# Kernel optimization log

Measured on AMD Instinct MI355X. Metric: run time of the kernel, lower is better.

## Reference

```python
import jax, jax.numpy as jnp
import numpy as np

H, D = 4, 32
DIM = H * D      # hidden_dim * heads = 128
L = 2            # num_layers
F = 1000         # functions per graph
BINS = 16
T = 16           # tensor_neurons
BOTT = 16        # bottle_neck_neurons


def _hgt(xd, xi, especs, Wk, bk, Wq, bq, Wv, bv, Wa, ba, sk, ar, mr, pr):
    # One HGTConv: per-type K/Q/V linears, per-relation head matrices a_rel/m_rel,
    # joint segment-softmax over all incoming edges per dst node, sum-aggregate,
    # gelu -> per-type out linear -> sigmoid-skip residual.
    xt = {"data": xd, "inst": xi}
    Ns = {"data": xd.shape[0], "inst": xi.shape[0]}
    ti = {"data": 0, "inst": 1}

    def proj(W, b):
        return {t: (xt[t] @ W[ti[t]] + b[ti[t]]).reshape(Ns[t], H, D) for t in xt}

    k, q, v = proj(Wk, bk), proj(Wq, bq), proj(Wv, bv)
    buckets = {"data": [], "inst": []}
    for st, dt, ei, r in especs:
        src, dst = ei[0], ei[1]
        krel = jnp.einsum("ehd,hdf->ehf", k[st][src], ar[r])        # [E,H,D]
        logit = (q[dt][dst] * krel).sum(-1) * (pr[r] / (D ** 0.5))   # [E,H]
        vrel = jnp.einsum("ehd,hdf->ehf", v[st][src], mr[r])        # [E,H,D]
        buckets[dt].append((logit, dst, vrel))
    out = {}
    for t in ("data", "inst"):
        logits = jnp.concatenate([b[0] for b in buckets[t]], 0)
        dst = jnp.concatenate([b[1] for b in buckets[t]], 0)
        msgs = jnp.concatenate([b[2] for b in buckets[t]], 0)
        mx = jax.lax.stop_gradient(jax.ops.segment_max(logits, dst, num_segments=Ns[t]))
        e = jnp.exp(logits - mx[dst])
        den = jax.ops.segment_sum(e, dst, num_segments=Ns[t])
        w = e / jnp.maximum(den[dst], 1e-16)
        agg = jax.ops.segment_sum(msgs * w[..., None], dst, num_segments=Ns[t]).reshape(Ns[t], DIM)
        o = jax.nn.gelu(agg) @ Wa[ti[t]] + ba[ti[t]]
        s = jax.nn.sigmoid(sk[ti[t]])
        out[t] = s * o + (1.0 - s) * xt[t]
    return out["data"], out["inst"]


def _conv_pass(xd, xi, edges, P):
    Wk, bk, Wq, bq, Wv, bv, Wa, ba, sk, ar, mr, pr = P
    ec, ein, eou, eca = edges
    for l in range(L):
        fe = [("inst", "inst", ec, 0), ("data", "inst", ein, 1),
              ("inst", "data", eou, 2), ("inst", "inst", eca, 3)]
        re = [("inst", "inst", ec[::-1], 0), ("inst", "data", ein[::-1], 1),
              ("data", "inst", eou[::-1], 2), ("inst", "inst", eca[::-1], 3)]
        p0 = [A[l, 0] for A in (Wk, bk, Wq, bq, Wv, bv, Wa, ba, sk, ar, mr, pr)]
        p1 = [A[l, 1] for A in (Wk, bk, Wq, bq, Wv, bv, Wa, ba, sk, ar, mr, pr)]
        d1, i1 = _hgt(xd, xi, fe, *p0)
        d2, i2 = _hgt(xd, xi, re, *p1)
        xd = jax.nn.relu(0.5 * d1 + 0.5 * d2)   # alpha = 0.5
        xi = jax.nn.relu(0.5 * i1 + 0.5 * i2)
    return xd, xi


def _att_pool(x, W_att):
    # SimGNN AttentionModule
    c = jnp.tanh(jnp.mean(x @ W_att, axis=0))
    s = jax.nn.sigmoid(x @ c)
    return x.T @ s  # [DIM]


def _func_pool(xd, xi, fd, fi, W_att):
    # per-function attention pooling via segment ops (cat(data,inst) per function)
    x = jnp.concatenate([xd, xi], 0)
    f = jnp.concatenate([fd, fi], 0)
    sums = jax.ops.segment_sum(x @ W_att, f, num_segments=F)
    cnt = jax.ops.segment_sum(jnp.ones((x.shape[0],), jnp.float32), f, num_segments=F)
    c = jnp.tanh(sums / jnp.maximum(cnt, 1.0)[:, None])
    s = jax.nn.sigmoid((x * c[f]).sum(-1))
    return jax.ops.segment_sum(x * s[:, None], f, num_segments=F)  # [F,DIM]


def _forward(g1_x_data, g1_x_inst, g2_x_data, g2_x_inst, W_k, b_k, W_q, b_q, W_v, b_v,
             W_a, b_a, skip, a_rel, m_rel, p_rel, W_att, W_tn, V_tn, b_tn, W_fc1, b_fc1,
             W_sc, b_sc, g1_ei_control, g1_ei_input, g1_ei_output, g1_ei_call,
             g1_func_data, g1_func_inst, g2_ei_control, g2_ei_input, g2_ei_output,
             g2_ei_call, g2_func_data, g2_func_inst):
    P = (W_k, b_k, W_q, b_q, W_v, b_v, W_a, b_a, skip, a_rel, m_rel, p_rel)
    d1, i1 = _conv_pass(g1_x_data, g1_x_inst, (g1_ei_control, g1_ei_input, g1_ei_output, g1_ei_call), P)
    d2, i2 = _conv_pass(g2_x_data, g2_x_inst, (g2_ei_control, g2_ei_input, g2_ei_output, g2_ei_call), P)
    f1 = _func_pool(d1, i1, g1_func_data, g1_func_inst, W_att)
    f2 = _func_pool(d2, i2, g2_func_data, g2_func_inst, W_att)
    # histogram of detached similarity scores (torch.histc over [min,max])
    sc = jax.lax.stop_gradient(f1 @ f2.T).reshape(-1)
    mn, mx = sc.min(), sc.max()
    idx = jnp.clip(jnp.floor((sc - mn) / jnp.maximum(mx - mn, 1e-12) * BINS).astype(jnp.int32), 0, BINS - 1)
    hist = jax.ops.segment_sum(jnp.ones_like(sc), idx, num_segments=BINS)
    hist = hist / hist.sum()
    p1 = _att_pool(jnp.concatenate([d1, i1], 0), W_att)
    p2 = _att_pool(jnp.concatenate([d2, i2], 0), W_att)
    scoring = jnp.einsum("i,ijk,j->k", p1, W_tn, p2)          # NTN bilinear [T]
    block = V_tn @ jnp.concatenate([p1, p2]) + b_tn
    tnet = jax.nn.relu(scoring + block)
    feats = jnp.concatenate([tnet, hist])[None, :]             # [1, T+BINS]
    h = jax.nn.relu(feats @ W_fc1 + b_fc1)
    return jax.nn.sigmoid(h @ W_sc + b_sc)                     # [1,1]


def setup_inputs():
    key = jax.random.key(0)
    ks = iter(jax.random.split(key, 80))
    Nd, Ni = 30000, 60000
    Ec, Ein, Eou, Eca = 120000, 90000, 90000, 30000

    def nrm(shape, s):
        return jax.random.normal(next(ks), shape, jnp.float32) * s

    def ri(n, hi):
        return jax.random.randint(next(ks), (n,), 0, hi, jnp.int32)

    inp = {}
    for g in ("g1", "g2"):
        inp[g + "_x_data"] = nrm((Nd, DIM), 1.0)
        inp[g + "_x_inst"] = nrm((Ni, DIM), 1.0)
        inp[g + "_ei_control"] = jnp.stack([ri(Ec, Ni), ri(Ec, Ni)])
        inp[g + "_ei_input"] = jnp.stack([ri(Ein, Nd), ri(Ein, Ni)])
        inp[g + "_ei_output"] = jnp.stack([ri(Eou, Ni), ri(Eou, Nd)])
        inp[g + "_ei_call"] = jnp.stack([ri(Eca, Ni), ri(Eca, Ni)])
        inp[g + "_func_data"] = (jnp.arange(Nd) % F).astype(jnp.int32)
        inp[g + "_func_inst"] = (jnp.arange(Ni) % F).astype(jnp.int32)
    w = 1.0 / (DIM ** 0.5)
    for nm in ("k", "q", "v", "a"):
        inp["W_" + nm] = nrm((L, 2, 2, DIM, DIM), w)
        inp["b_" + nm] = jnp.zeros((L, 2, 2, DIM), jnp.float32)
    inp["skip"] = jnp.ones((L, 2, 2), jnp.float32)
    inp["a_rel"] = nrm((L, 2, 4, H, D, D), 1.0 / (D ** 0.5))
    inp["m_rel"] = nrm((L, 2, 4, H, D, D), 1.0 / (D ** 0.5))
    inp["p_rel"] = jnp.ones((L, 2, 4, H), jnp.float32)
    inp["W_att"] = nrm((DIM, DIM), w)
    inp["W_tn"] = nrm((DIM, DIM, T), w)
    inp["V_tn"] = nrm((T, 2 * DIM), w)
    inp["b_tn"] = jnp.zeros((T,), jnp.float32)
    inp["W_fc1"] = nrm((T + BINS, BOTT), 0.1)
    inp["b_fc1"] = jnp.zeros((BOTT,), jnp.float32)
    inp["W_sc"] = nrm((BOTT, 1), 0.1)
    inp["b_sc"] = jnp.zeros((1,), jnp.float32)
    return inp


def reference(g1_x_data, g1_x_inst, g2_x_data, g2_x_inst, W_k, b_k, W_q, b_q, W_v, b_v,
              W_a, b_a, skip, a_rel, m_rel, p_rel, W_att, W_tn, V_tn, b_tn, W_fc1, b_fc1,
              W_sc, b_sc, g1_ei_control, g1_ei_input, g1_ei_output, g1_ei_call,
              g1_func_data, g1_func_inst, g2_ei_control, g2_ei_input, g2_ei_output,
              g2_ei_call, g2_func_data, g2_func_inst):
    return _forward(g1_x_data, g1_x_inst, g2_x_data, g2_x_inst, W_k, b_k, W_q, b_q, W_v, b_v,
                    W_a, b_a, skip, a_rel, m_rel, p_rel, W_att, W_tn, V_tn, b_tn, W_fc1, b_fc1,
                    W_sc, b_sc, g1_ei_control, g1_ei_input, g1_ei_output, g1_ei_call,
                    g1_func_data, g1_func_inst, g2_ei_control, g2_ei_input, g2_ei_output,
                    g2_ei_call, g2_func_data, g2_func_inst)
```

## Files before the change

### kernel.cpp

```cpp
#include <hip/hip_runtime.h>
#include <math.h>

#define FFUNC 1000

typedef __attribute__((ext_vector_type(8))) short s8v;
typedef __attribute__((ext_vector_type(4))) float f4v;

__device__ __forceinline__ float sigf(float x){ return 1.0f/(1.0f+__expf(-x)); }
__device__ __forceinline__ float geluf(float x){
  float u = 1.5957691216057308f * (x + 0.044715f*x*x*x);
  return x / (1.0f + __expf(-u));
}
__device__ __forceinline__ unsigned fkey(float f){
  unsigned u = __float_as_uint(f);
  return (u & 0x80000000u) ? ~u : (u | 0x80000000u);
}
__device__ __forceinline__ float funkey(unsigned k){
  unsigned u = (k & 0x80000000u) ? (k ^ 0x80000000u) : ~k;
  return __uint_as_float(u);
}
__device__ __forceinline__ void atomAddF(float* p, float v){ unsafeAtomicAdd(p, v); }
__device__ __forceinline__ unsigned short bfr(float x){
  unsigned u = __float_as_uint(x);
  unsigned r = (u + 0x7FFFu + ((u >> 16) & 1u)) >> 16;
  return (unsigned short)r;
}
__device__ __forceinline__ float b2f(unsigned short v){
  return __uint_as_float((unsigned)v << 16);
}

__global__ void packw_k(const float* __restrict__ W, unsigned short* __restrict__ out){
  int mat = blockIdx.x;
  const float* w = W + (size_t)mat*16384;
  unsigned short* o = out + (size_t)mat*16384;
  for (int u=0; u<64; u++){
    int oi = u*256 + threadIdx.x;
    int j = oi & 7, l = (oi>>3) & 63, nt = (oi>>9) & 7, kt = oi >> 12;
    float v = w[(size_t)(kt*32 + 8*(l>>4) + j)*128 + nt*16 + (l&15)];
    o[oi] = bfr(v);
  }
}

__global__ void packa_k(const float* __restrict__ A, unsigned short* __restrict__ out){
  int ent = blockIdx.x;
  const float* a = A + (size_t)ent*4096;
  unsigned short* o = out + (size_t)ent*4096;
  for (int u=0; u<16; u++){
    int oi = u*256 + threadIdx.x;
    int j = oi & 7, l = (oi>>3) & 63, nt = (oi>>9) & 1, h = oi >> 10;
    float v = a[(size_t)h*1024 + (size_t)(8*(l>>4)+j)*32 + nt*16 + (l&15)];
    o[oi] = bfr(v);
  }
}

struct KX { int styp[4]; int koff[4]; };
__global__ __launch_bounds__(256) void gemm_kqvx_k(
    const void* __restrict__ xdv, const void* __restrict__ xiv, int af32,
    int nd, int ni, int gbd,
    const unsigned short* __restrict__ WK, const unsigned short* __restrict__ WQ,
    const unsigned short* __restrict__ WV,
    const float* __restrict__ bK, const float* __restrict__ bQ, const float* __restrict__ bV,
    const unsigned short* __restrict__ ARpc, const unsigned short* __restrict__ MRpc,
    unsigned short* __restrict__ Qb,
    unsigned short* __restrict__ KRK, unsigned short* __restrict__ KRV, KX kx)
{
  __shared__ __align__(16) unsigned short tile[64*128];
  int blk = blockIdx.x;
  int ty = (blk >= gbd);
  int N = ty ? ni : nd;
  int rbase = (ty ? (blk - gbd) : blk) * 64;
  size_t obase = ty ? (size_t)nd*128 : 0;
  const unsigned short* wk = WK + (ty ? 16384 : 0);
  const unsigned short* wq = WQ + (ty ? 16384 : 0);
  const unsigned short* wv = WV + (ty ? 16384 : 0);
  const float* bk2 = bK + (ty ? 128 : 0);
  const float* bq2 = bQ + (ty ? 128 : 0);
  const float* bv2 = bV + (ty ? 128 : 0);
  const float* Af = (const float*)(ty ? xiv : xdv);
  const unsigned short* Ab = (const unsigned short*)(ty ? xiv : xdv);

  int t = threadIdx.x;
  int l = t & 63, w = t >> 6, b = l >> 4, m = l & 15;
  int arow = rbase + w*16 + m;
  bool rv = arow < N;
  int lrow = w*16 + m;

  s8v axf[4];
  #pragma unroll
  for (int kt=0; kt<4; kt++){
    s8v af = (s8v){0,0,0,0,0,0,0,0};
    if (rv){
      if (af32){
        const float* ap = Af + (size_t)arow*128 + kt*32 + b*8;
        float4 x0 = *(const float4*)ap;
        float4 x1 = *(const float4*)(ap + 4);
        af[0]=(short)bfr(x0.x); af[1]=(short)bfr(x0.y); af[2]=(short)bfr(x0.z); af[3]=(short)bfr(x0.w);
        af[4]=(short)bfr(x1.x); af[5]=(short)bfr(x1.y); af[6]=(short)bfr(x1.z); af[7]=(short)bfr(x1.w);
      } else {
        af = *(const s8v*)(Ab + (size_t)arow*128 + kt*32 + b*8);
      }
    }
    axf[kt] = af;
  }

  f4v acc[8];
  #pragma unroll
  for (int nt=0; nt<8; nt++) acc[nt] = (f4v){0,0,0,0};
  #pragma unroll
  for (int kt=0; kt<4; kt++)
    #pragma unroll
    for (int nt=0; nt<8; nt++){
      s8v bf = *(const s8v*)(wq + ((kt*8 + nt)*64 + l)*8);
      acc[nt] = __builtin_amdgcn_mfma_f32_16x16x32_bf16(axf[kt], bf, acc[nt], 0, 0, 0);
    }
  #pragma unroll
  for (int r2=0; r2<4; r2++){
    int trow = w*16 + 4*b + r2;
    #pragma unroll
    for (int nt=0; nt<8; nt++){
      int col = nt*16 + m;
      int ch = (col>>3) ^ (trow&15);
      tile[trow*128 + ch*8 + (col&7)] = bfr(acc[nt][r2] + bq2[col]);
    }
  }
  __syncthreads();
  #pragma unroll
  for (int it=0; it<4; it++){
    int idx = it*256 + t;
    int rr = idx >> 4, cc = idx & 15;
    int orow = rbase + rr;
    if (orow < N)
      *(uint4*)(Qb + obase + (size_t)orow*128 + cc*8) =
          *(const uint4*)(&tile[rr*128 + ((cc ^ (rr&15))*8)]);
  }
  __syncthreads();

  #pragma unroll
  for (int nt=0; nt<8; nt++) acc[nt] = (f4v){0,0,0,0};
  #pragma unroll
  for (int kt=0; kt<4; kt++)
    #pragma unroll
    for (int nt=0; nt<8; nt++){
      s8v bf = *(const s8v*)(wk + ((kt*8 + nt)*64 + l)*8);
      acc[nt] = __builtin_amdgcn_mfma_f32_16x16x32_bf16(axf[kt], bf, acc[nt], 0, 0, 0);
    }
  #pragma unroll
  for (int r2=0; r2<4; r2++){
    int trow = w*16 + 4*b + r2;
    #pragma unroll
    for (int nt=0; nt<8; nt++){
      int col = nt*16 + m;
      int ch = (col>>3) ^ (trow&15);
      tile[trow*128 + ch*8 + (col&7)] = bfr(acc[nt][r2] + bk2[col]);
    }
  }
  __syncthreads();
  {
    s8v kf[4];
    #pragma unroll
    for (int h=0; h<4; h++){
      int ch = (h*4 + b) ^ (lrow&15);
      kf[h] = *(const s8v*)(&tile[lrow*128 + ch*8]);
    }
    __syncthreads();
    #pragma unroll
    for (int r=0; r<4; r++){
      if (kx.styp[r] != ty) continue;
      const unsigned short* Ap = ARpc + r*4096;
      f4v xa[8];
      #pragma unroll
      for (int i=0;i<8;i++) xa[i] = (f4v){0,0,0,0};
      #pragma unroll
      for (int h=0; h<4; h++)
        #pragma unroll
        for (int n2=0; n2<2; n2++){
          s8v bf = *(const s8v*)(Ap + ((h*2 + n2)*64 + l)*8);
          xa[h*2+n2] = __builtin_amdgcn_mfma_f32_16x16x32_bf16(kf[h], bf, xa[h*2+n2], 0, 0, 0);
        }
      #pragma unroll
      for (int r2=0; r2<4; r2++){
        int trow = w*16 + 4*b + r2;
        #pragma unroll
        for (int h=0; h<4; h++)
          #pragma unroll
          for (int n2=0; n2<2; n2++){
            int col = h*32 + n2*16 + m;
            int ch = (col>>3) ^ (trow&15);
            tile[trow*128 + ch*8 + (col&7)] = bfr(xa[h*2+n2][r2]);
          }
      }
      __syncthreads();
      int ko = kx.koff[r];
      #pragma unroll
      for (int it=0; it<4; it++){
        int idx = it*256 + t;
        int rr = idx >> 4, cc = idx & 15;
        int orow = rbase + rr;
        if (orow < N)
          *(uint4*)(KRK + (size_t)(ko + orow)*128 + cc*8) =
              *(const uint4*)(&tile[rr*128 + ((cc ^ (rr&15))*8)]);
      }
      __syncthreads();
    }
  }

  #pragma unroll
  for (int nt=0; nt<8; nt++) acc[nt] = (f4v){0,0,0,0};
  #pragma unroll
  for (int kt=0; kt<4; kt++)
    #pragma unroll
    for (int nt=0; nt<8; nt++){
      s8v bf = *(const s8v*)(wv + ((kt*8 + nt)*64 + l)*8);
      acc[nt] = __builtin_amdgcn_mfma_f32_16x16x32_bf16(axf[kt], bf, acc[nt], 0, 0, 0);
    }
  #pragma unroll
  for (int r2=0; r2<4; r2++){
    int trow = w*16 + 4*b + r2;
    #pragma unroll
    for (int nt=0; nt<8; nt++){
      int col = nt*16 + m;
      int ch = (col>>3) ^ (trow&15);
      tile[trow*128 + ch*8 + (col&7)] = bfr(acc[nt][r2] + bv2[col]);
    }
  }
  __syncthreads();
  {
    s8v vf[4];
    #pragma unroll
    for (int h=0; h<4; h++){
      int ch = (h*4 + b) ^ (lrow&15);
      vf[h] = *(const s8v*)(&tile[lrow*128 + ch*8]);
    }
    __syncthreads();
    #pragma unroll
    for (int r=0; r<4; r++){
      if (kx.styp[r] != ty) continue;
      const unsigned short* Ap = MRpc + r*4096;
      f4v xa[8];
      #pragma unroll
      for (int i=0;i<8;i++) xa[i] = (f4v){0,0,0,0};
      #pragma unroll
      for (int h=0; h<4; h++)
        #pragma unroll
        for (int n2=0; n2<2; n2++){
          s8v bf = *(const s8v*)(Ap + ((h*2 + n2)*64 + l)*8);
          xa[h*2+n2] = __builtin_amdgcn_mfma_f32_16x16x32_bf16(vf[h], bf, xa[h*2+n2], 0, 0, 0);
        }
      #pragma unroll
      for (int r2=0; r2<4; r2++){
        int trow = w*16 + 4*b + r2;
        #pragma unroll
        for (int h=0; h<4; h++)
          #pragma unroll
          for (int n2=0; n2<2; n2++){
            int col = h*32 + n2*16 + m;
            int ch = (col>>3) ^ (trow&15);
            tile[trow*128 + ch*8 + (col&7)] = bfr(xa[h*2+n2][r2]);
          }
      }
      __syncthreads();
      int ko = kx.koff[r];
      #pragma unroll
      for (int it=0; it<4; it++){
        int idx = it*256 + t;
        int rr = idx >> 4, cc = idx & 15;
        int orow = rbase + rr;
        if (orow < N)
          *(uint4*)(KRV + (size_t)(ko + orow)*128 + cc*8) =
              *(const uint4*)(&tile[rr*128 + ((cc ^ (rr&15))*8)]);
      }
      __syncthreads();
    }
  }
}

__global__ __launch_bounds__(256) void gemm_epi_k(
    const unsigned short* __restrict__ AGGb, const float* __restrict__ DENb,
    int nd, int ni, int gbd,
    const unsigned short* __restrict__ WA, const float* __restrict__ bA,
    const void* __restrict__ xin_dv, const void* __restrict__ xin_iv, int xf32,
    const unsigned short* __restrict__ o1p, unsigned short* __restrict__ out,
    const float* __restrict__ skp, int mode)
{
  __shared__ __align__(16) float ftile[64*128];
  int blk = blockIdx.x;
  int ty = (blk >= gbd);
  int N = ty ? ni : nd;
  int rbase = (ty ? (blk - gbd) : blk) * 64;
  int goff = ty ? nd : 0;
  const unsigned short* wa = WA + (ty ? 16384 : 0);
  const float* ba2 = bA + (ty ? 128 : 0);
  const float* xinF = (const float*)(ty ? xin_iv : xin_dv);
  const unsigned short* xinB = (const unsigned short*)(ty ? xin_iv : xin_dv);
  float s = sigf(skp[ty]), s1 = 1.0f - s;

  int t = threadIdx.x;
  int l = t & 63, w = t >> 6, b = l >> 4, m = l & 15;
  int arow = rbase + w*16 + m;
  bool rv = arow < N;
  f4v acc[8];
  #pragma unroll
  for (int nt=0; nt<8; nt++) acc[nt] = (f4v){0,0,0,0};

  float4 dv4 = make_float4(1.f,1.f,1.f,1.f);
  if (rv){
    size_t grow = (size_t)(goff + arow);
    float4 dr = *(const float4*)(DENb + grow*4);
    dv4.x = 1.0f / fmaxf(dr.x, 1e-16f);
    dv4.y = 1.0f / fmaxf(dr.y, 1e-16f);
    dv4.z = 1.0f / fmaxf(dr.z, 1e-16f);
    dv4.w = 1.0f / fmaxf(dr.w, 1e-16f);
  }
  #pragma unroll
  for (int kt=0; kt<4; kt++){
    s8v af = (s8v){0,0,0,0,0,0,0,0};
    if (rv){
      size_t grow = (size_t)(goff + arow);
      float dv = (kt==0)?dv4.x:(kt==1)?dv4.y:(kt==2)?dv4.z:dv4.w;
      s8v ag = *(const s8v*)(AGGb + grow*128 + kt*32 + b*8);
      #pragma unroll
      for (int jj=0; jj<8; jj++)
        af[jj] = (short)bfr(geluf(b2f((unsigned short)ag[jj]) * dv));
    }
    #pragma unroll
    for (int nt=0; nt<8; nt++){
      s8v bf = *(const s8v*)(wa + ((kt*8 + nt)*64 + l)*8);
      acc[nt] = __builtin_amdgcn_mfma_f32_16x16x32_bf16(af, bf, acc[nt], 0, 0, 0);
    }
  }
  #pragma unroll
  for (int r2=0; r2<4; r2++){
    int trow = w*16 + 4*b + r2;
    #pragma unroll
    for (int nt=0; nt<8; nt++){
      int col = nt*16 + m;
      int ch = (col>>2) ^ (trow&31);
      ftile[trow*128 + ch*4 + (col&3)] = acc[nt][r2];
    }
  }
  __syncthreads();
  #pragma unroll
  for (int it=0; it<8; it++){
    int idx = it*256 + t;
    int rr = idx >> 5, cc = idx & 31;
    int orow = rbase + rr;
    if (orow >= N) continue;
    size_t grow = (size_t)(goff + orow);
    float4 a4 = *(const float4*)(&ftile[rr*128 + ((cc ^ (rr&31))*4)]);
    float4 b4 = *(const float4*)(ba2 + cc*4);
    float xv0, xv1, xv2, xv3;
    if (xf32){
      float4 x4 = *(const float4*)(xinF + (size_t)orow*128 + cc*4);
      xv0=x4.x; xv1=x4.y; xv2=x4.z; xv3=x4.w;
    } else {
      ushort4 x4 = *(const ushort4*)(xinB + (size_t)orow*128 + cc*4);
      xv0=b2f(x4.x); xv1=b2f(x4.y); xv2=b2f(x4.z); xv3=b2f(x4.w);
    }
    float v0 = s*(a4.x + b4.x) + s1*xv0;
    float v1 = s*(a4.y + b4.y) + s1*xv1;
    float v2 = s*(a4.z + b4.z) + s1*xv2;
    float v3 = s*(a4.w + b4.w) + s1*xv3;
    if (mode == 3){
      ushort4 o4 = *(const ushort4*)(o1p + grow*128 + cc*4);
      v0 = fmaxf(0.5f*b2f(o4.x) + 0.5f*v0, 0.f);
      v1 = fmaxf(0.5f*b2f(o4.y) + 0.5f*v1, 0.f);
      v2 = fmaxf(0.5f*b2f(o4.z) + 0.5f*v2, 0.f);
      v3 = fmaxf(0.5f*b2f(o4.w) + 0.5f*v3, 0.f);
    }
    *(ushort4*)(out + grow*128 + cc*4) =
        make_ushort4(bfr(v0), bfr(v1), bfr(v2), bfr(v3));
  }
}

struct ScanDesc { int n[8]; };

struct HD {
  int blk0[9];
  const int* dst[8];
  const int* src[8];
  int E[8];
  int cnto[8];
  int permo[8];
};
__global__ void csr_hist_all_k(HD d, int* __restrict__ cnt){
  int b = blockIdx.x;
  int r = 0;
  while (r < 7 && b >= d.blk0[r+1]) r++;
  int e = (b - d.blk0[r])*256 + threadIdx.x;
  if (e < d.E[r]) atomicAdd(&cnt[d.cnto[r] + d.dst[r][e]], 1);
}
__global__ void csr_fill_all_k(HD d, int* __restrict__ curs, int* __restrict__ perm){
  int b = blockIdx.x;
  int r = 0;
  while (r < 7 && b >= d.blk0[r+1]) r++;
  int e = (b - d.blk0[r])*256 + threadIdx.x;
  if (e < d.E[r]){
    int pos = atomicAdd(&curs[d.cnto[r] + d.dst[r][e]], 1);
    perm[d.permo[r] + pos] = d.src[r][e] | ((r & 3) << 24);
  }
}

__global__ __launch_bounds__(1024) void scan_p1(ScanDesc sd, const int* __restrict__ offs,
                                                int* __restrict__ part, int NO, int MAXT){
  int ent = blockIdx.y, tile = blockIdx.x;
  int n = sd.n[ent];
  int i = tile*1024 + threadIdx.x;
  int v = (i < n) ? offs[(size_t)ent*NO + i] : 0;
  #pragma unroll
  for (int d2=1; d2<64; d2<<=1) v += __shfl_xor(v, d2, 64);
  __shared__ int ws_[16];
  int lane = threadIdx.x & 63, wv = threadIdx.x >> 6;
  if (lane == 0) ws_[wv] = v;
  __syncthreads();
  if (threadIdx.x == 0){
    int s = 0;
    #pragma unroll
    for (int k=0;k<16;k++) s += ws_[k];
    part[ent*MAXT + tile] = s;
  }
}

__global__ __launch_bounds__(1024) void scan_p2(int* __restrict__ part, int MAXT, int nent){
  int tid = threadIdx.x, lane = tid & 63, wv = tid >> 6;
  __shared__ int wsum[16];
  __shared__ int woff[17];
  for (int ent=0; ent<nent; ent++){
    int v = (tid < MAXT) ? part[ent*MAXT + tid] : 0;
    int s = v;
    #pragma unroll
    for (int d2=1; d2<64; d2<<=1){
      int t2 = __shfl_up(s, d2, 64);
      if (lane >= d2) s += t2;
    }
    if (lane == 63) wsum[wv] = s;
    __syncthreads();
    if (wv == 0 && lane < 16){
      int x = wsum[lane];
      #pragma unroll
      for (int d2=1; d2<16; d2<<=1){
        int t2 = __shfl_up(x, d2, 64);
        if (lane >= d2) x += t2;
      }
      woff[lane+1] = x;
      if (lane == 0) woff[0] = 0;
    }
    __syncthreads();
    if (tid < MAXT) part[ent*MAXT + tid] = woff[wv] + s - v;
    __syncthreads();
  }
}

__global__ __launch_bounds__(1024) void scan_p3(ScanDesc sd, int* __restrict__ offs,
                                                int* __restrict__ curs,
                                                const int* __restrict__ part, int NO, int MAXT){
  int ent = blockIdx.y, tile = blockIdx.x;
  int n = sd.n[ent];
  int i = tile*1024 + threadIdx.x;
  int v = (i < n) ? offs[(size_t)ent*NO + i] : 0;
  int lane = threadIdx.x & 63, wv = threadIdx.x >> 6;
  int s = v;
  #pragma unroll
  for (int d2=1; d2<64; d2<<=1){
    int t2 = __shfl_up(s, d2, 64);
    if (lane >= d2) s += t2;
  }
  __shared__ int wsum[16];
  __shared__ int woff[17];
  if (lane == 63) wsum[wv] = s;
  __syncthreads();
  if (wv == 0 && lane < 16){
    int x = wsum[lane];
    #pragma unroll
    for (int d2=1; d2<16; d2<<=1){
      int t2 = __shfl_up(x, d2, 64);
      if (lane >= d2) x += t2;
    }
    woff[lane+1] = x;
    if (lane == 0) woff[0] = 0;
  }
  __syncthreads();
  int excl = part[ent*MAXT + tile] + woff[wv] + s - v;
  if (i < n){
    offs[(size_t)ent*NO + i] = excl;
    curs[(size_t)ent*NO + i] = excl;
  }
  if (i == n-1) offs[(size_t)ent*NO + n] = excl + v;
}

__global__ void fhist_k(const int* __restrict__ fd, const int* __restrict__ fi,
                        int Nd, int Ni, int* __restrict__ cnt){
  int nt = Nd + Ni;
  for (int n = blockIdx.x*256 + threadIdx.x; n < nt; n += gridDim.x*256){
    int f = (n < Nd) ? fd[n] : fi[n-Nd];
    atomicAdd(&cnt[f], 1);
  }
}
__global__ void ffill_k(const int* __restrict__ fd, const int* __restrict__ fi,
                        int Nd, int Ni, int* __restrict__ curs, int* __restrict__ perm){
  int nt = Nd + Ni;
  for (int n = blockIdx.x*256 + threadIdx.x; n < nt; n += gridDim.x*256){
    int f = (n < Nd) ? fd[n] : fi[n-Nd];
    int pos = atomicAdd(&curs[f], 1);
    perm[pos] = n;
  }
}

struct MD { int koff[4]; };
__global__ __launch_bounds__(256) void e12m_k(
    const unsigned short* __restrict__ KRK, const unsigned short* __restrict__ KRV,
    const unsigned short* __restrict__ Qb,
    const int* __restrict__ offs, const int* __restrict__ perm, int nrows,
    const float* __restrict__ pr,
    unsigned short* __restrict__ aggb, float* __restrict__ den, MD md)
{
  int gidx = blockIdx.x*256 + threadIdx.x;
  int node = gidx >> 5; if (node >= nrows) return;
  int sub = gidx & 31, h = sub >> 3, j = sub & 7;
  int o0 = offs[node], o1 = offs[node+1];
  unsigned short* ap = aggb + (size_t)node*128 + h*32 + j*4;
  if (o0 == o1){
    *(ushort4*)ap = make_ushort4(0,0,0,0);
    if (j == 0) den[(size_t)node*4 + h] = 0.f;
    return;
  }
  ushort4 qa = *(const ushort4*)(Qb + (size_t)node*128 + h*32 + j*4);
  float q0=b2f(qa.x), q1=b2f(qa.y), q2=b2f(qa.z), q3=b2f(qa.w);
  float scl[4];
  #pragma unroll
  for (int r=0;r<4;r++) scl[r] = pr[r*4 + h] * 0.17677669529663687f;
  float mx = -INFINITY, ds = 0.f;
  float4 acc = make_float4(0.f,0.f,0.f,0.f);
  for (int i=o0; i<o1; ++i){
    int pk = perm[i];
    int src = pk & 0xFFFFFF, rel = pk >> 24;
    size_t rowo = (size_t)(md.koff[rel] + src)*128 + h*32 + j*4;
    ushort4 aa = *(const ushort4*)(KRK + rowo);
    ushort4 vv = *(const ushort4*)(KRV + rowo);
    float p = b2f(aa.x)*q0 + b2f(aa.y)*q1 + b2f(aa.z)*q2 + b2f(aa.w)*q3;
    p += __shfl_xor(p, 1, 8);
    p += __shfl_xor(p, 2, 8);
    p += __shfl_xor(p, 4, 8);
    float lg = p * scl[rel];
    float nm = fmaxf(mx, lg);
    float corr = __expf(mx - nm);
    float ev = __expf(lg - nm);
    acc.x = acc.x*corr + ev*b2f(vv.x);
    acc.y = acc.y*corr + ev*b2f(vv.y);
    acc.z = acc.z*corr + ev*b2f(vv.z);
    acc.w = acc.w*corr + ev*b2f(vv.w);
    ds = ds*corr + ev;
    mx = nm;
  }
  *(ushort4*)ap = make_ushort4(bfr(acc.x), bfr(acc.y), bfr(acc.z), bfr(acc.w));
  if (j == 0) den[(size_t)node*4 + h] = ds;
}

__global__ __launch_bounds__(256) void gemmb_k(
    const float* __restrict__ A, int N,
    const unsigned short* __restrict__ Wp, const float* __restrict__ bias,
    float* __restrict__ outf, int mode, const float* __restrict__ rdiv)
{
  int t = threadIdx.x;
  int l = t & 63, w = t >> 6, b = l >> 4, m = l & 15;
  int arow = blockIdx.x*64 + w*16 + m;
  bool rv = arow < N;
  float dv = 1.0f;
  if (rv && rdiv) dv = 1.0f / fmaxf(rdiv[arow], 1.0f);
  f4v acc[8];
  #pragma unroll
  for (int nt=0; nt<8; nt++) acc[nt] = (f4v){0,0,0,0};
  #pragma unroll
  for (int kt=0; kt<4; kt++){
    s8v af = (s8v){0,0,0,0,0,0,0,0};
    if (rv){
      const float* ap = A + (size_t)arow*128 + kt*32 + b*8;
      float4 x0 = *(const float4*)ap;
      float4 x1 = *(const float4*)(ap + 4);
      af[0]=(short)bfr(x0.x*dv); af[1]=(short)bfr(x0.y*dv); af[2]=(short)bfr(x0.z*dv); af[3]=(short)bfr(x0.w*dv);
      af[4]=(short)bfr(x1.x*dv); af[5]=(short)bfr(x1.y*dv); af[6]=(short)bfr(x1.z*dv); af[7]=(short)bfr(x1.w*dv);
    }
    #pragma unroll
    for (int nt=0; nt<8; nt++){
      s8v bf = *(const s8v*)(Wp + ((kt*8 + nt)*64 + l)*8);
      acc[nt] = __builtin_amdgcn_mfma_f32_16x16x32_bf16(af, bf, acc[nt], 0, 0, 0);
    }
  }
  #pragma unroll
  for (int r2=0; r2<4; r2++){
    int orow = blockIdx.x*64 + w*16 + 4*b + r2;
    if (orow >= N) continue;
    #pragma unroll
    for (int nt=0; nt<8; nt++){
      int col = nt*16 + m;
      float v = acc[nt][r2];
      if (bias) v += bias[col];
      if (mode == 1) v = tanhf(v);
      outf[(size_t)orow*128 + col] = v;
    }
  }
}

__global__ __launch_bounds__(256) void f1c_k(const unsigned short* __restrict__ X,
    const int* __restrict__ foffs, const int* __restrict__ fperm,
    float* __restrict__ fsum, float* __restrict__ fcnt)
{
  __shared__ __align__(16) float red[4][128];
  int t = threadIdx.x, wv = t >> 6, lane = t & 63;
  int f = blockIdx.x;
  int o0 = foffs[f], o1 = foffs[f+1];
  float a0 = 0, a1 = 0;
  for (int i = o0 + wv; i < o1; i += 4){
    ushort2 x = *(const ushort2*)(X + (size_t)fperm[i]*128 + lane*2);
    a0 += b2f(x.x); a1 += b2f(x.y);
  }
  red[wv][lane*2] = a0; red[wv][lane*2+1] = a1;
  __syncthreads();
  if (t < 128)
    fsum[(size_t)f*128 + t] = red[0][t] + red[1][t] + red[2][t] + red[3][t];
  if (t == 0) fcnt[f] = (float)(o1 - o0);
}

__global__ __launch_bounds__(256) void f23c_k(const unsigned short* __restrict__ X,
    const int* __restrict__ foffs, const int* __restrict__ fperm,
    const float* __restrict__ cf, const float* __restrict__ attc,
    unsigned short* __restrict__ fembb, float* __restrict__ pooled)
{
  __shared__ __align__(16) float rede[4][128];
  __shared__ __align__(16) float redp[4][128];
  int t = threadIdx.x, wv = t >> 6, lane = t & 63;
  int f = blockIdx.x;
  int o0 = foffs[f], o1 = foffs[f+1];
  float c0 = cf[(size_t)f*128 + lane*2], c1 = cf[(size_t)f*128 + lane*2 + 1];
// ... 141 lines not shown
  float acc = 0;
  for (int i = pr_*8; i < pr_*8+8; ++i){
    float pi = P1[i];
    const float* wrow = Wtn + ((size_t)i*128)*16 + k;
    float a2 = 0;
    for (int j=0;j<128;++j) a2 += P2[j]*wrow[(size_t)j*16];
    acc += pi*a2;
  }
  part[t] = acc;
  __syncthreads();
  if (t < 16){
    float sc_ = 0;
    for (int p=0;p<16;p++) sc_ += part[p*16 + t];
    float bl = btn[t];
    for (int j=0;j<256;j++) bl += Vtn[(size_t)t*256 + j] * (j<128 ? P1[j] : P2[j-128]);
    float tv = sc_ + bl;
    feats[t] = tv > 0.f ? tv : 0.f;
    feats[16+t] = (float)hist[t] * (1.0f/((float)FFUNC*(float)FFUNC));
  }
  __syncthreads();
  if (t < 16){
    float a2 = bfc1[t];
    for (int q2=0;q2<32;q2++) a2 += feats[q2]*Wfc1[q2*16 + t];
    hv[t] = a2 > 0.f ? a2 : 0.f;
  }
  __syncthreads();
  if (t == 0){
    float z = bsc[0];
    for (int m=0;m<16;m++) z += hv[m]*Wsc[m];
    outp[0] = sigf(z);
  }
}

extern "C" void kernel_launch(void* const* d_in, const int* in_sizes, int n_in,
                              void* d_out, int out_size, void* d_ws, size_t ws_size,
                              hipStream_t stream)
{
  (void)n_in; (void)out_size; (void)ws_size;
  const float* Wk = (const float*)d_in[16];
  const float* bk = (const float*)d_in[17];
  const float* Wq = (const float*)d_in[18];
  const float* bq = (const float*)d_in[19];
  const float* Wv = (const float*)d_in[20];
  const float* bv = (const float*)d_in[21];
  const float* Wa = (const float*)d_in[22];
  const float* ba = (const float*)d_in[23];
  const float* SKp = (const float*)d_in[24];
  const float* AR = (const float*)d_in[25];
  const float* MRm = (const float*)d_in[26];
  const float* PRp = (const float*)d_in[27];
  const float* WATT = (const float*)d_in[28];
  const float* WTN = (const float*)d_in[29];
  const float* VTN = (const float*)d_in[30];
  const float* BTN = (const float*)d_in[31];
  const float* WFC1 = (const float*)d_in[32];
  const float* BFC1 = (const float*)d_in[33];
  const float* WSC = (const float*)d_in[34];
  const float* BSC = (const float*)d_in[35];

  int NdA[2] = { in_sizes[0]/128, in_sizes[8]/128 };
  int NiA[2] = { in_sizes[1]/128, in_sizes[9]/128 };
  int EA[2][4];
  for (int g=0; g<2; g++)
    for (int r=0; r<4; r++) EA[g][r] = in_sizes[g*8+2+r]/2;

  int NdM = NdA[0] > NdA[1] ? NdA[0] : NdA[1];
  int NiM = NiA[0] > NiA[1] ? NiA[0] : NiA[1];
  long EtotM = 0;
  for (int g=0; g<2; g++){
    long et = 0; for (int r=0;r<4;r++) et += EA[g][r];
    if (et > EtotM) EtotM = et;
  }
  size_t nrowsM = (size_t)NdM + (size_t)NiM;
  int NOR = (int)(((nrowsM + 2 + 63)/64)*64);
  long KR4rows = 3L*NiM + NdM;

  char* wp = (char*)d_ws;
  auto alloc = [&](size_t bytes)->void*{
    void* p = (void*)wp;
    wp += (bytes + 255) & ~(size_t)255;
    return p;
  };
  unsigned short* Xb   = (unsigned short*)alloc(nrowsM*128*2);
  unsigned short* AGGb = (unsigned short*)alloc(nrowsM*128*2);
  float*          DEN  = (float*)alloc(nrowsM*4*4);
  unsigned short* O1b  = (unsigned short*)alloc(nrowsM*128*2);
  unsigned short* Qb   = (unsigned short*)alloc(nrowsM*128*2);
  unsigned short* KRK  = (unsigned short*)alloc((size_t)KR4rows*128*2);
  unsigned short* KRV  = (unsigned short*)alloc((size_t)KR4rows*128*2);
  int*            OFFS3= (int*)alloc((size_t)3*NOR*4);
  int*            PERM = (int*)alloc((size_t)2*EtotM*4);
  int*            FPERM= (int*)alloc(nrowsM*4);
  int*            PART = (int*)alloc((size_t)3*1024*4);
  float*          GS[2];
  GS[0] = (float*)alloc((size_t)257280*4);
  GS[1] = (float*)alloc((size_t)257280*4);
  unsigned short* FB[2];
  FB[0] = (unsigned short*)alloc((size_t)FFUNC*128*2);
  FB[1] = (unsigned short*)alloc((size_t)FFUNC*128*2);
  unsigned*       MM   = (unsigned*)alloc(2*4);
  unsigned*       HIST = (unsigned*)alloc(16*4);
  unsigned short* WKP  = (unsigned short*)alloc((size_t)8*16384*2);
  unsigned short* WQP  = (unsigned short*)alloc((size_t)8*16384*2);
  unsigned short* WVP  = (unsigned short*)alloc((size_t)8*16384*2);
  unsigned short* WAP  = (unsigned short*)alloc((size_t)8*16384*2);
  unsigned short* WATTP= (unsigned short*)alloc((size_t)16384*2);
  unsigned short* ARP  = (unsigned short*)alloc((size_t)16*4096*2);
  unsigned short* MRP  = (unsigned short*)alloc((size_t)16*4096*2);
  size_t uni_bytes = (size_t)FFUNC*FFUNC*4;
  size_t curs_bytes = (size_t)3*NOR*4;
  void* UNI = alloc(uni_bytes > curs_bytes ? uni_bytes : curs_bytes);
  int*   CURS3 = (int*)UNI;
  float* SCb   = (float*)UNI;

  packw_k<<<8,256,0,stream>>>(Wk, WKP);
  packw_k<<<8,256,0,stream>>>(Wq, WQP);
  packw_k<<<8,256,0,stream>>>(Wv, WVP);
  packw_k<<<8,256,0,stream>>>(Wa, WAP);
  packw_k<<<1,256,0,stream>>>(WATT, WATTP);
  packa_k<<<16,256,0,stream>>>(AR, ARP);
  packa_k<<<16,256,0,stream>>>(MRm, MRP);

  const size_t OF_FSUM=0, OF_FCNT=128000, OF_CF=129024, OF_ATTC=257024, OF_POOL=257152;
  const int stf[4] = {1,0,1,1};
  const int dtf[4] = {1,1,0,1};

  for (int g=0; g<2; ++g){
    int nd = NdA[g], ni = NiA[g];
    int nrows = nd + ni;
    int E[4] = {EA[g][0],EA[g][1],EA[g][2],EA[g][3]};
    const int* ei[4] = {(const int*)d_in[g*8+2], (const int*)d_in[g*8+3],
                        (const int*)d_in[g*8+4], (const int*)d_in[g*8+5]};
    const int* fdp = (const int*)d_in[g*8+6];
    const int* fip = (const int*)d_in[g*8+7];
    const float* x0d = (const float*)d_in[g*8+0];
    const float* x0i = (const float*)d_in[g*8+1];
    int gbd = (nd+63)/64, gbi = (ni+63)/64;
    int nb = gbd + gbi;
    int ntb = (nrows+255)/256; if (ntb > 2048) ntb = 2048;

    int koff[2][4], stA[2][4], dtA[2][4];
    for (int c=0;c<2;c++){
      int run = 0;
      for (int r=0;r<4;r++){
        stA[c][r] = (c==0) ? stf[r] : dtf[r];
        dtA[c][r] = (c==0) ? dtf[r] : stf[r];
        koff[c][r] = run;
        run += stA[c][r] ? ni : nd;
      }
    }

    hipMemsetAsync(OFFS3, 0, (size_t)3*NOR*4, stream);
    HD hd; int hb = 0;
    for (int c2=0; c2<2; c2++)
      for (int r=0; r<4; r++){
        int ent = c2*4 + r;
        hd.blk0[ent] = hb;
        hd.dst[ent] = (c2==0) ? ei[r]+E[r] : ei[r];
        hd.src[ent] = (c2==0) ? ei[r] : ei[r]+E[r];
        hd.E[ent] = E[r];
        hd.cnto[ent] = c2*NOR + (dtA[c2][r] ? nd : 0);
        hd.permo[ent] = c2*(int)EtotM;
        hb += (E[r]+255)/256;
      }
    hd.blk0[8] = hb;
    csr_hist_all_k<<<hb,256,0,stream>>>(hd, OFFS3);
    fhist_k<<<ntb,256,0,stream>>>(fdp, fip, nd, ni, OFFS3 + (size_t)2*NOR);
    ScanDesc sd; sd.n[0] = nrows; sd.n[1] = nrows; sd.n[2] = FFUNC;
    int maxtiles = (nrows + 1023)/1024; if (maxtiles < 1) maxtiles = 1;
    dim3 sgrid(maxtiles, 3);
    scan_p1<<<sgrid,1024,0,stream>>>(sd, OFFS3, PART, NOR, maxtiles);
    scan_p2<<<1,1024,0,stream>>>(PART, maxtiles, 3);
    scan_p3<<<sgrid,1024,0,stream>>>(sd, OFFS3, CURS3, PART, NOR, maxtiles);
    csr_fill_all_k<<<hb,256,0,stream>>>(hd, CURS3, PERM);
    ffill_k<<<ntb,256,0,stream>>>(fdp, fip, nd, ni, CURS3 + (size_t)2*NOR, FPERM);

    for (int l=0; l<2; ++l){
      const void* xd = (l==0) ? (const void*)x0d : (const void*)Xb;
      const void* xi = (l==0) ? (const void*)x0i : (const void*)(Xb + (size_t)nd*128);
      int af32 = (l==0);
      for (int c=0; c<2; ++c){
        int pc = l*2 + c;
        KX kx;
        for (int r=0;r<4;r++){ kx.styp[r] = stA[c][r]; kx.koff[r] = koff[c][r]; }
        gemm_kqvx_k<<<nb,256,0,stream>>>(
            xd, xi, af32, nd, ni, gbd,
            WKP+(size_t)pc*2*16384, WQP+(size_t)pc*2*16384, WVP+(size_t)pc*2*16384,
            bk+(size_t)pc*2*128, bq+(size_t)pc*2*128, bv+(size_t)pc*2*128,
            ARP + (size_t)pc*4*4096, MRP + (size_t)pc*4*4096,
            Qb, KRK, KRV, kx);
        MD md;
        for (int r=0;r<4;r++) md.koff[r] = koff[c][r];
        int eblk = (nrows*32 + 255)/256;
        e12m_k<<<eblk,256,0,stream>>>(KRK, KRV, Qb,
                                      OFFS3 + (size_t)c*NOR, PERM + (size_t)c*EtotM, nrows,
                                      PRp + (size_t)pc*16, AGGb, DEN, md);
        gemm_epi_k<<<nb,256,0,stream>>>(
            AGGb, DEN, nd, ni, gbd,
            WAP+(size_t)pc*2*16384, ba+(size_t)pc*2*128,
            xd, xi, af32,
            (c==1) ? O1b : (const unsigned short*)nullptr,
            (c==0) ? O1b : Xb,
            SKp + (size_t)pc*2, (c==0) ? 2 : 3);
      }
    }
    float* fsum = GS[g]+OF_FSUM;  float* fcnt = GS[g]+OF_FCNT;
    float* cf   = GS[g]+OF_CF;    float* attc = GS[g]+OF_ATTC;
    float* pool = GS[g]+OF_POOL;
    hipMemsetAsync(pool, 0, 128*4, stream);
    f1c_k<<<FFUNC,256,0,stream>>>(Xb, OFFS3 + (size_t)2*NOR, FPERM, fsum, fcnt);
    attc2_k<<<1,1024,0,stream>>>(fsum, 1.0f/(float)nrows, WATT, attc);
    gemmb_k<<<(FFUNC+63)/64,256,0,stream>>>(fsum, FFUNC, WATTP, nullptr, cf, 1, fcnt);
    f23c_k<<<FFUNC,256,0,stream>>>(Xb, OFFS3 + (size_t)2*NOR, FPERM, cf, attc, FB[g], pool);
  }
  hist_init_k<<<1,32,0,stream>>>(MM, HIST);
  dim3 gnt((FFUNC+63)/64, (FFUNC+63)/64);
  gemmnt_b<<<gnt,256,0,stream>>>(FB[0], FB[1], SCb, MM);
  hist_k<<<512,256,0,stream>>>(SCb, MM, HIST);
  final_k<<<1,256,0,stream>>>(GS[0]+OF_POOL, GS[1]+OF_POOL, WTN, VTN, BTN, HIST,
                              WFC1, BFC1, WSC, BSC, (float*)d_out);
}
```

Baseline: 1.764 ms.

## Store relation K/V in FP8 and fuse both direction epilogues into one kernel

The relation-transformed K and V rows, which the edge kernel gathers once per edge, are now stored as 8-bit e4m3-style values instead of bf16. This halves gather traffic at the cost of precision. Separately, the two per-direction out-projection epilogues are merged into one kernel that computes both GEMMs and the averaged ReLU combine. This drops one launch and the O1 intermediate round trip per layer, but needs separate AGG/DEN buffers for each direction. The FP8 rounding could hurt accuracy relative to the reference.

```diff
diff --git a/kernel.cpp b/kernel.cpp
--- a/kernel.cpp
+++ b/kernel.cpp
@@ -27,6 +27,22 @@
 }
 __device__ __forceinline__ float b2f(unsigned short v){
   return __uint_as_float((unsigned)v << 16);
+}
+__device__ __forceinline__ unsigned char f2fp8(float x){
+  unsigned u = __float_as_uint(x);
+  unsigned s = (u >> 24) & 0x80u;
+  unsigned au = u & 0x7FFFFFFFu;
+  if (au > 0x43E00000u) au = 0x43E00000u;
+  unsigned r = au + 0x7FFFFu + ((au >> 20) & 1u);
+  int e8 = (int)(r >> 23) - 120;
+  if (e8 <= 0) return (unsigned char)s;
+  return (unsigned char)(s | (e8 << 3) | ((r >> 20) & 7u));
+}
+__device__ __forceinline__ float fp82f(unsigned c){
+  unsigned s = (c & 0x80u) << 24;
+  unsigned em = c & 0x7Fu;
+  unsigned f = s | (((em >> 3) + 120u) << 23) | ((em & 7u) << 20);
+  return (em < 8u) ? __uint_as_float(s) : __uint_as_float(f);
 }
 
 __global__ void packw_k(const float* __restrict__ W, unsigned short* __restrict__ out){
@@ -62,9 +78,10 @@
     const float* __restrict__ bK, const float* __restrict__ bQ, const float* __restrict__ bV,
     const unsigned short* __restrict__ ARpc, const unsigned short* __restrict__ MRpc,
     unsigned short* __restrict__ Qb,
-    unsigned short* __restrict__ KRK, unsigned short* __restrict__ KRV, KX kx)
+    unsigned char* __restrict__ KRK, unsigned char* __restrict__ KRV, KX kx)
 {
   __shared__ __align__(16) unsigned short tile[64*128];
+  unsigned char* tb = (unsigned char*)tile;
   int blk = blockIdx.x;
   int ty = (blk >= gbd);
   int N = ty ? ni : nd;
@@ -183,22 +200,19 @@
         #pragma unroll
         for (int h=0; h<4; h++)
           #pragma unroll
-          for (int n2=0; n2<2; n2++){
-            int col = h*32 + n2*16 + m;
-            int ch = (col>>3) ^ (trow&15);
-            tile[trow*128 + ch*8 + (col&7)] = bfr(xa[h*2+n2][r2]);
-          }
+          for (int n2=0; n2<2; n2++)
+            tb[trow*128 + h*32 + n2*16 + m] = f2fp8(xa[h*2+n2][r2]);
       }
       __syncthreads();
       int ko = kx.koff[r];
       #pragma unroll
-      for (int it=0; it<4; it++){
+      for (int it=0; it<2; it++){
         int idx = it*256 + t;
-        int rr = idx >> 4, cc = idx & 15;
+        int rr = idx >> 3, cc = idx & 7;
         int orow = rbase + rr;
         if (orow < N)
-          *(uint4*)(KRK + (size_t)(ko + orow)*128 + cc*8) =
-              *(const uint4*)(&tile[rr*128 + ((cc ^ (rr&15))*8)]);
+          *(uint4*)(KRK + (size_t)(ko + orow)*128 + cc*16) =
+              *(const uint4*)(tb + rr*128 + cc*16);
       }
       __syncthreads();
     }
@@ -252,123 +266,146 @@
         #pragma unroll
         for (int h=0; h<4; h++)
           #pragma unroll
-          for (int n2=0; n2<2; n2++){
-            int col = h*32 + n2*16 + m;
-            int ch = (col>>3) ^ (trow&15);
-            tile[trow*128 + ch*8 + (col&7)] = bfr(xa[h*2+n2][r2]);
-          }
+          for (int n2=0; n2<2; n2++)
+            tb[trow*128 + h*32 + n2*16 + m] = f2fp8(xa[h*2+n2][r2]);
       }
       __syncthreads();
       int ko = kx.koff[r];
       #pragma unroll
-      for (int it=0; it<4; it++){
+      for (int it=0; it<2; it++){
         int idx = it*256 + t;
-        int rr = idx >> 4, cc = idx & 15;
+        int rr = idx >> 3, cc = idx & 7;
         int orow = rbase + rr;
         if (orow < N)
-          *(uint4*)(KRV + (size_t)(ko + orow)*128 + cc*8) =
-              *(const uint4*)(&tile[rr*128 + ((cc ^ (rr&15))*8)]);
+          *(uint4*)(KRV + (size_t)(ko + orow)*128 + cc*16) =
+              *(const uint4*)(tb + rr*128 + cc*16);
       }
       __syncthreads();
     }
   }
 }
 
-__global__ __launch_bounds__(256) void gemm_epi_k(
-    const unsigned short* __restrict__ AGGb, const float* __restrict__ DENb,
+__global__ __launch_bounds__(256) void gemm_epi2_k(
+    const unsigned short* __restrict__ AGG0, const float* __restrict__ DEN0,
+    const unsigned short* __restrict__ AGG1, const float* __restrict__ DEN1,
     int nd, int ni, int gbd,
-    const unsigned short* __restrict__ WA, const float* __restrict__ bA,
+    const unsigned short* __restrict__ WAb, const float* __restrict__ bAb,
     const void* __restrict__ xin_dv, const void* __restrict__ xin_iv, int xf32,
-    const unsigned short* __restrict__ o1p, unsigned short* __restrict__ out,
-    const float* __restrict__ skp, int mode)
+    unsigned short* __restrict__ out, const float* __restrict__ skp)
 {
-  __shared__ __align__(16) float ftile[64*128];
+  __shared__ __align__(16) unsigned short tA[64*128];
+  __shared__ __align__(16) unsigned short tB[64*128];
   int blk = blockIdx.x;
   int ty = (blk >= gbd);
   int N = ty ? ni : nd;
   int rbase = (ty ? (blk - gbd) : blk) * 64;
   int goff = ty ? nd : 0;
-  const unsigned short* wa = WA + (ty ? 16384 : 0);
-  const float* ba2 = bA + (ty ? 128 : 0);
+  const unsigned short* wa0 = WAb + (size_t)ty*16384;
+  const unsigned short* wa1 = WAb + (size_t)(2+ty)*16384;
+  const float* ba0 = bAb + ty*128;
+  const float* ba1 = bAb + (2+ty)*128;
   const float* xinF = (const float*)(ty ? xin_iv : xin_dv);
   const unsigned short* xinB = (const unsigned short*)(ty ? xin_iv : xin_dv);
-  float s = sigf(skp[ty]), s1 = 1.0f - s;
+  float s0 = sigf(skp[ty]),     s0c = 1.0f - s0;
+  float s1 = sigf(skp[2 + ty]), s1c = 1.0f - s1;
 
   int t = threadIdx.x;
   int l = t & 63, w = t >> 6, b = l >> 4, m = l & 15;
   int arow = rbase + w*16 + m;
   bool rv = arow < N;
-  f4v acc[8];
-  #pragma unroll
-  for (int nt=0; nt<8; nt++) acc[nt] = (f4v){0,0,0,0};
-
-  float4 dv4 = make_float4(1.f,1.f,1.f,1.f);
-  if (rv){
-    size_t grow = (size_t)(goff + arow);
-    float4 dr = *(const float4*)(DENb + grow*4);
-    dv4.x = 1.0f / fmaxf(dr.x, 1e-16f);
-    dv4.y = 1.0f / fmaxf(dr.y, 1e-16f);
-    dv4.z = 1.0f / fmaxf(dr.z, 1e-16f);
-    dv4.w = 1.0f / fmaxf(dr.w, 1e-16f);
-  }
-  #pragma unroll
-  for (int kt=0; kt<4; kt++){
-    s8v af = (s8v){0,0,0,0,0,0,0,0};
+  size_t grow = (size_t)(goff + (rv ? arow : 0));
+
+  #pragma unroll
+  for (int dir=0; dir<2; dir++){
+    const unsigned short* AG = dir ? AGG1 : AGG0;
+    const float* DN = dir ? DEN1 : DEN0;
+    const unsigned short* wa = dir ? wa1 : wa0;
+    unsigned short* tl = dir ? tB : tA;
+    f4v acc[8];
+    #pragma unroll
+    for (int nt=0; nt<8; nt++) acc[nt] = (f4v){0,0,0,0};
+    float4 dv4 = make_float4(1.f,1.f,1.f,1.f);
     if (rv){
-      size_t grow = (size_t)(goff + arow);
-      float dv = (kt==0)?dv4.x:(kt==1)?dv4.y:(kt==2)?dv4.z:dv4.w;
-      s8v ag = *(const s8v*)(AGGb + grow*128 + kt*32 + b*8);
+      float4 dr = *(const float4*)(DN + grow*4);
+      dv4.x = 1.0f / fmaxf(dr.x, 1e-16f);
+      dv4.y = 1.0f / fmaxf(dr.y, 1e-16f);
+      dv4.z = 1.0f / fmaxf(dr.z, 1e-16f);
+      dv4.w = 1.0f / fmaxf(dr.w, 1e-16f);
+    }
+    #pragma unroll
+    for (int kt=0; kt<4; kt++){
+      s8v af = (s8v){0,0,0,0,0,0,0,0};
+      if (rv){
+        float dv = (kt==0)?dv4.x:(kt==1)?dv4.y:(kt==2)?dv4.z:dv4.w;
+        s8v ag = *(const s8v*)(AG + grow*128 + kt*32 + b*8);
+        #pragma unroll
+        for (int jj=0; jj<8; jj++)
+          af[jj] = (short)bfr(geluf(b2f((unsigned short)ag[jj]) * dv));
+      }
       #pragma unroll
-      for (int jj=0; jj<8; jj++)
-        af[jj] = (short)bfr(geluf(b2f((unsigned short)ag[jj]) * dv));
-    }
-    #pragma unroll
-    for (int nt=0; nt<8; nt++){
-      s8v bf = *(const s8v*)(wa + ((kt*8 + nt)*64 + l)*8);
-      acc[nt] = __builtin_amdgcn_mfma_f32_16x16x32_bf16(af, bf, acc[nt], 0, 0, 0);
-    }
-  }
-  #pragma unroll
-  for (int r2=0; r2<4; r2++){
-    int trow = w*16 + 4*b + r2;
-    #pragma unroll
-    for (int nt=0; nt<8; nt++){
-      int col = nt*16 + m;
-      int ch = (col>>2) ^ (trow&31);
-      ftile[trow*128 + ch*4 + (col&3)] = acc[nt][r2];
-    }
-  }
-  __syncthreads();
-  #pragma unroll
-  for (int it=0; it<8; it++){
+      for (int nt=0; nt<8; nt++){
+        s8v bf = *(const s8v*)(wa + ((kt*8 + nt)*64 + l)*8);
+        acc[nt] = __builtin_amdgcn_mfma_f32_16x16x32_bf16(af, bf, acc[nt], 0, 0, 0);
+      }
+    }
+    #pragma unroll
+    for (int r2=0; r2<4; r2++){
+      int trow = w*16 + 4*b + r2;
+      #pragma unroll
+      for (int nt=0; nt<8; nt++){
+        int col = nt*16 + m;
+        int ch = (col>>3) ^ (trow&15);
+        tl[trow*128 + ch*8 + (col&7)] = bfr(acc[nt][r2]);
+      }
+    }
+  }
+  __syncthreads();
+  #pragma unroll
+  for (int it=0; it<4; it++){
     int idx = it*256 + t;
-    int rr = idx >> 5, cc = idx & 31;
+    int rr = idx >> 4, cc = idx & 15;
     int orow = rbase + rr;
     if (orow >= N) continue;
-    size_t grow = (size_t)(goff + orow);
-    float4 a4 = *(const float4*)(&ftile[rr*128 + ((cc ^ (rr&31))*4)]);
-    float4 b4 = *(const float4*)(ba2 + cc*4);
-    float xv0, xv1, xv2, xv3;
+    size_t gr = (size_t)(goff + orow);
+    int so = rr*128 + ((cc ^ (rr&15))*8);
+    float a0[8], a1[8];
+    {
+      ushort4 p0 = *(const ushort4*)(&tA[so]);
+      ushort4 p1 = *(const ushort4*)(&tA[so+4]);
+      a0[0]=b2f(p0.x); a0[1]=b2f(p0.y); a0[2]=b2f(p0.z); a0[3]=b2f(p0.w);
+      a0[4]=b2f(p1.x); a0[5]=b2f(p1.y); a0[6]=b2f(p1.z); a0[7]=b2f(p1.w);
+      ushort4 q0 = *(const ushort4*)(&tB[so]);
+      ushort4 q1 = *(const ushort4*)(&tB[so+4]);
+      a1[0]=b2f(q0.x); a1[1]=b2f(q0.y); a1[2]=b2f(q0.z); a1[3]=b2f(q0.w);
+      a1[4]=b2f(q1.x); a1[5]=b2f(q1.y); a1[6]=b2f(q1.z); a1[7]=b2f(q1.w);
+    }
+    int c0 = cc*8;
+    float4 b00 = *(const float4*)(ba0 + c0);
+    float4 b01 = *(const float4*)(ba0 + c0 + 4);
+    float4 b10 = *(const float4*)(ba1 + c0);
+    float4 b11 = *(const float4*)(ba1 + c0 + 4);
+    float bb0[8] = {b00.x,b00.y,b00.z,b00.w,b01.x,b01.y,b01.z,b01.w};
+    float bb1[8] = {b10.x,b10.y,b10.z,b10.w,b11.x,b11.y,b11.z,b11.w};
+    float xv[8];
     if (xf32){
-      float4 x4 = *(const float4*)(xinF + (size_t)orow*128 + cc*4);
-      xv0=x4.x; xv1=x4.y; xv2=x4.z; xv3=x4.w;
+      float4 x0 = *(const float4*)(xinF + (size_t)orow*128 + c0);
+      float4 x1 = *(const float4*)(xinF + (size_t)orow*128 + c0 + 4);
+      xv[0]=x0.x; xv[1]=x0.y; xv[2]=x0.z; xv[3]=x0.w;
+      xv[4]=x1.x; xv[5]=x1.y; xv[6]=x1.z; xv[7]=x1.w;
     } else {
-      ushort4 x4 = *(const ushort4*)(xinB + (size_t)orow*128 + cc*4);
-      xv0=b2f(x4.x); xv1=b2f(x4.y); xv2=b2f(x4.z); xv3=b2f(x4.w);
-    }
-    float v0 = s*(a4.x + b4.x) + s1*xv0;
-    float v1 = s*(a4.y + b4.y) + s1*xv1;
-    float v2 = s*(a4.z + b4.z) + s1*xv2;
-    float v3 = s*(a4.w + b4.w) + s1*xv3;
-    if (mode == 3){
-      ushort4 o4 = *(const ushort4*)(o1p + grow*128 + cc*4);
-      v0 = fmaxf(0.5f*b2f(o4.x) + 0.5f*v0, 0.f);
-      v1 = fmaxf(0.5f*b2f(o4.y) + 0.5f*v1, 0.f);
-      v2 = fmaxf(0.5f*b2f(o4.z) + 0.5f*v2, 0.f);
-      v3 = fmaxf(0.5f*b2f(o4.w) + 0.5f*v3, 0.f);
-    }
-    *(ushort4*)(out + grow*128 + cc*4) =
-        make_ushort4(bfr(v0), bfr(v1), bfr(v2), bfr(v3));
+      ushort4 x0 = *(const ushort4*)(xinB + (size_t)orow*128 + c0);
+      ushort4 x1 = *(const ushort4*)(xinB + (size_t)orow*128 + c0 + 4);
+      xv[0]=b2f(x0.x); xv[1]=b2f(x0.y); xv[2]=b2f(x0.z); xv[3]=b2f(x0.w);
+      xv[4]=b2f(x1.x); xv[5]=b2f(x1.y); xv[6]=b2f(x1.z); xv[7]=b2f(x1.w);
+    }
+    unsigned short ov[8];
+    #pragma unroll
+    for (int q=0; q<8; q++){
+      float o1 = s0*(a0[q] + bb0[q]) + s0c*xv[q];
+      float o2 = s1*(a1[q] + bb1[q]) + s1c*xv[q];
+      ov[q] = bfr(fmaxf(0.5f*o1 + 0.5f*o2, 0.f));
+    }
+    *(uint4*)(out + gr*128 + c0) = *(const uint4*)ov;
   }
 }
 
@@ -507,7 +544,7 @@
 
 struct MD { int koff[4]; };
 __global__ __launch_bounds__(256) void e12m_k(
-    const unsigned short* __restrict__ KRK, const unsigned short* __restrict__ KRV,
+    const unsigned char* __restrict__ KRK, const unsigned char* __restrict__ KRV,
     const unsigned short* __restrict__ Qb,
     const int* __restrict__ offs, const int* __restrict__ perm, int nrows,
     const float* __restrict__ pr,
@@ -534,9 +571,10 @@
     int pk = perm[i];
     int src = pk & 0xFFFFFF, rel = pk >> 24;
     size_t rowo = (size_t)(md.koff[rel] + src)*128 + h*32 + j*4;
-    ushort4 aa = *(const ushort4*)(KRK + rowo);
-    ushort4 vv = *(const ushort4*)(KRV + rowo);
-    float p = b2f(aa.x)*q0 + b2f(aa.y)*q1 + b2f(aa.z)*q2 + b2f(aa.w)*q3;
+    unsigned ku = *(const unsigned*)(KRK + rowo);
+    unsigned vu = *(const unsigned*)(KRV + rowo);
+    float p = fp82f(ku & 255u)*q0 + fp82f((ku>>8)&255u)*q1
+            + fp82f((ku>>16)&255u)*q2 + fp82f(ku>>24)*q3;
     p += __shfl_xor(p, 1, 8);
     p += __shfl_xor(p, 2, 8);
     p += __shfl_xor(p, 4, 8);
@@ -544,10 +582,10 @@
     float nm = fmaxf(mx, lg);
     float corr = __expf(mx - nm);
     float ev = __expf(lg - nm);
-    acc.x = acc.x*corr + ev*b2f(vv.x);
-    acc.y = acc.y*corr + ev*b2f(vv.y);
-    acc.z = acc.z*corr + ev*b2f(vv.z);
-    acc.w = acc.w*corr + ev*b2f(vv.w);
+    acc.x = acc.x*corr + ev*fp82f(vu & 255u);
+    acc.y = acc.y*corr + ev*fp82f((vu>>8)&255u);
+    acc.z = acc.z*corr + ev*fp82f((vu>>16)&255u);
+    acc.w = acc.w*corr + ev*fp82f(vu>>24);
     ds = ds*corr + ev;
     mx = nm;
   }
@@ -855,12 +893,13 @@
     return p;
   };
   unsigned short* Xb   = (unsigned short*)alloc(nrowsM*128*2);
-  unsigned short* AGGb = (unsigned short*)alloc(nrowsM*128*2);
-  float*          DEN  = (float*)alloc(nrowsM*4*4);
-  unsigned short* O1b  = (unsigned short*)alloc(nrowsM*128*2);
+  unsigned short* AGG0 = (unsigned short*)alloc(nrowsM*128*2);
+  unsigned short* AGG1 = (unsigned short*)alloc(nrowsM*128*2);
+  float*          DEN0 = (float*)alloc(nrowsM*4*4);
+  float*          DEN1 = (float*)alloc(nrowsM*4*4);
   unsigned short* Qb   = (unsigned short*)alloc(nrowsM*128*2);
-  unsigned short* KRK  = (unsigned short*)alloc((size_t)KR4rows*128*2);
-  unsigned short* KRV  = (unsigned short*)alloc((size_t)KR4rows*128*2);
+  unsigned char*  KRK8 = (unsigned char*)alloc((size_t)KR4rows*128);
+  unsigned char*  KRV8 = (unsigned char*)alloc((size_t)KR4rows*128);
   int*            OFFS3= (int*)alloc((size_t)3*NOR*4);
   int*            PERM = (int*)alloc((size_t)2*EtotM*4);
   int*            FPERM= (int*)alloc(nrowsM*4);
@@ -961,21 +1000,20 @@
             WKP+(size_t)pc*2*16384, WQP+(size_t)pc*2*16384, WVP+(size_t)pc*2*16384,
             bk+(size_t)pc*2*128, bq+(size_t)pc*2*128, bv+(size_t)pc*2*128,
             ARP + (size_t)pc*4*4096, MRP + (size_t)pc*4*4096,
-            Qb, KRK, KRV, kx);
+            Qb, KRK8, KRV8, kx);
         MD md;
         for (int r=0;r<4;r++) md.koff[r] = koff[c][r];
         int eblk = (nrows*32 + 255)/256;
-        e12m_k<<<eblk,256,0,stream>>>(KRK, KRV, Qb,
+        e12m_k<<<eblk,256,0,stream>>>(KRK8, KRV8, Qb,
                                       OFFS3 + (size_t)c*NOR, PERM + (size_t)c*EtotM, nrows,
-                                      PRp + (size_t)pc*16, AGGb, DEN, md);
-        gemm_epi_k<<<nb,256,0,stream>>>(
-            AGGb, DEN, nd, ni, gbd,
-            WAP+(size_t)pc*2*16384, ba+(size_t)pc*2*128,
-            xd, xi, af32,
-            (c==1) ? O1b : (const unsigned short*)nullptr,
-            (c==0) ? O1b : Xb,
-            SKp + (size_t)pc*2, (c==0) ? 2 : 3);
-      }
+                                      PRp + (size_t)pc*16,
+                                      (c==0) ? AGG0 : AGG1,
+                                      (c==0) ? DEN0 : DEN1, md);
+      }
+      gemm_epi2_k<<<nb,256,0,stream>>>(
+          AGG0, DEN0, AGG1, DEN1, nd, ni, gbd,
+          WAP + (size_t)l*4*16384, ba + (size_t)l*4*128,
+          xd, xi, af32, Xb, SKp + (size_t)l*4);
     }
     float* fsum = GS[g]+OF_FSUM;  float* fcnt = GS[g]+OF_FCNT;
     float* cf   = GS[g]+OF_CF;    float* attc = GS[g]+OF_ATTC;
```

Measured after the change: 1.873 ms. 1.06x slower.
